# Kernel optimization log

Measured on AMD Instinct MI355X. Metric: run time of the kernel, lower is better.

Reference implementation:

```python
import jax, jax.numpy as jnp
import numpy as np

D_MODEL = 768
D_HEAD = 64
BATCH = 2
SEQ = 4096


def setup_inputs() -> dict:
    key = jax.random.key(0)
    k1, k2, k3, k4, k5 = jax.random.split(key, 5)
    x = jax.random.normal(k1, (BATCH, SEQ, D_MODEL), dtype=jnp.float32)
    # causal mask as the module expects: (seq_len, seq_len) float, 1 where attend allowed
    mask = jnp.tril(jnp.ones((SEQ, SEQ), dtype=jnp.float32))
    # weights initialized like the module: randn / sqrt(d_model)
    scale = 1.0 / np.sqrt(D_MODEL)
    Wq = jax.random.normal(k2, (D_HEAD, D_MODEL), dtype=jnp.float32) * scale
    Wk = jax.random.normal(k3, (D_HEAD, D_MODEL), dtype=jnp.float32) * scale
    Wv = jax.random.normal(k4, (D_HEAD, D_MODEL), dtype=jnp.float32) * scale
    Wo = jax.random.normal(k5, (D_MODEL, D_HEAD), dtype=jnp.float32) * scale
    return {"x": x, "mask": mask, "Wq": Wq, "Wk": Wk, "Wv": Wv, "Wo": Wo}


def reference(x, mask, Wq, Wk, Wv, Wo):
    # q,k,v: (B, S, d_head); Linear with weight (out,in) => x @ W.T
    q = jnp.einsum('bsm,hm->bsh', x, Wq)
    k = jnp.einsum('bsm,hm->bsh', x, Wk)
    v = jnp.einsum('bsm,hm->bsh', x, Wv)
    scores = jnp.einsum('bqd,bkd->bqk', q, k) / np.sqrt(D_HEAD)  # (B,S,S)
    seq_len = x.shape[1]
    m = mask[:seq_len, :seq_len]
    # faithful to the torch code: tril(scores) - 1e10 * (1 - mask)
    scores = jnp.tril(scores) - 1e10 * (1.0 - m)
    attn = jax.nn.softmax(scores, axis=-1)
    z = jnp.einsum('bqk,bkd->bqd', attn, v)  # (B,S,d_head)
    out = jnp.einsum('bsh,mh->bsm', z, Wo)   # (B,S,d_model)
    return out
```

## Files before the change

### kernel.cpp

```cpp
#include <hip/hip_runtime.h>
#include <stdint.h>

#define SEQ 4096
#define DM 768
#define DH 64

typedef __attribute__((ext_vector_type(8))) short short8;
typedef __attribute__((ext_vector_type(4))) short short4v;
typedef __attribute__((ext_vector_type(4))) float f32x4;
typedef __attribute__((ext_vector_type(2))) uint32_t uint2v;

#define LOG2E 1.4426950408889634f

static __device__ __forceinline__ short bf16r(float f) {
  union { float f; uint32_t u; } v; v.f = f;
  uint32_t u = v.u;
  return (short)((u + 0x7FFFu + ((u >> 16) & 1u)) >> 16);
}

static __device__ __forceinline__ float bf16f(uint16_t u) {
  union { uint32_t u; float f; } v; v.u = ((uint32_t)u) << 16;
  return v.f;
}

static __device__ __forceinline__ uint32_t cvtpk(float a, float b) {
  uint32_t r;
  asm("v_cvt_pk_bf16_f32 %0, %1, %2" : "=v"(r) : "v"(a), "v"(b));
  return r;
}

static __device__ __forceinline__ int swz(int row, int b) {
  return row * 128 + (b ^ ((row & 7) << 4));
}

__global__ __launch_bounds__(256) void qkv_proj(
    const float* __restrict__ x, const float* __restrict__ Wq,
    const float* __restrict__ Wk, const float* __restrict__ Wv,
    uint16_t* __restrict__ qg, uint16_t* __restrict__ kg, uint16_t* __restrict__ vg) {
  __shared__ char smem[49152] __attribute__((aligned(16)));
  const int tid = threadIdx.x;
  const int lane = tid & 63, wv = tid >> 6;
  const int l15 = lane & 15, l4 = lane >> 4;
  const int row0 = blockIdx.x * 32;
  const int nh = blockIdx.y;

  const int xr = tid >> 4, xc4 = tid & 15;
  const int mh = wv & 1, ng = wv >> 1;
  const int wr0 = tid >> 3, wb16 = tid & 7;

  const float* xp0 = x + (size_t)(row0 + xr) * DM + xc4 * 4;
  const float* xp1 = x + (size_t)(row0 + 16 + xr) * DM + xc4 * 4;

  const float* wp[3];
  int wlds[3];
  #pragma unroll
  for (int i = 0; i < 3; ++i) {
    int grow = nh * 96 + wr0 + i * 32;
    wp[i] = (grow < 64) ? (Wq + (size_t)grow * DM)
          : (grow < 128) ? (Wk + (size_t)(grow - 64) * DM)
                         : (Wv + (size_t)(grow - 128) * DM);
    wlds[i] = 4096 + swz(wr0 + i * 32, wb16 * 16);
  }
  const int xlds0 = swz(xr, xc4 * 8), xlds1 = swz(xr + 16, xc4 * 8);

  f32x4 acc[3];
  #pragma unroll
  for (int j = 0; j < 3; ++j) acc[j] = (f32x4){0.f, 0.f, 0.f, 0.f};

  float4 xA0, xA1, xB0, xB1;
  float4 wA[3][2], wB[3][2];

#define ISSUE_A(K0)                                                              \
  { xA0 = *(const float4*)(xp0 + (K0)); xA1 = *(const float4*)(xp1 + (K0));      \
    _Pragma("unroll")                                                            \
    for (int i = 0; i < 3; ++i) {                                                \
      wA[i][0] = *(const float4*)(wp[i] + (K0) + wb16 * 8);                      \
      wA[i][1] = *(const float4*)(wp[i] + (K0) + wb16 * 8 + 4);                  \
    }                                                                            \
    __builtin_amdgcn_sched_barrier(0); }
#define ISSUE_B(K0)                                                              \
  { xB0 = *(const float4*)(xp0 + (K0)); xB1 = *(const float4*)(xp1 + (K0));      \
    _Pragma("unroll")                                                            \
    for (int i = 0; i < 3; ++i) {                                                \
      wB[i][0] = *(const float4*)(wp[i] + (K0) + wb16 * 8);                      \
      wB[i][1] = *(const float4*)(wp[i] + (K0) + wb16 * 8 + 4);                  \
    }                                                                            \
    __builtin_amdgcn_sched_barrier(0); }
#define WRITE_SET(X0, X1, WS, BUF)                                               \
  { char* base_ = smem + (BUF) * 16384;                                          \
    uint2v p0 = { cvtpk(X0.x, X0.y), cvtpk(X0.z, X0.w) };                        \
    *(uint2v*)(base_ + xlds0) = p0;                                              \
    uint2v p1 = { cvtpk(X1.x, X1.y), cvtpk(X1.z, X1.w) };                        \
    *(uint2v*)(base_ + xlds1) = p1;                                              \
    _Pragma("unroll")                                                            \
    for (int i = 0; i < 3; ++i) {                                                \
      union { uint32_t u[4]; short8 s; } pk;                                     \
      pk.u[0] = cvtpk(WS[i][0].x, WS[i][0].y);                                   \
      pk.u[1] = cvtpk(WS[i][0].z, WS[i][0].w);                                   \
      pk.u[2] = cvtpk(WS[i][1].x, WS[i][1].y);                                   \
      pk.u[3] = cvtpk(WS[i][1].z, WS[i][1].w);                                   \
      *(short8*)(base_ + wlds[i]) = pk.s;                                        \
    } }
#define COMPUTE(BUF)                                                             \
  { char* base_ = smem + (BUF) * 16384;                                          \
    _Pragma("unroll")                                                            \
    for (int kc = 0; kc < 2; ++kc) {                                             \
      short8 af = *(const short8*)(base_ + swz(mh * 16 + l15, kc * 64 + l4 * 16)); \
      _Pragma("unroll")                                                          \
      for (int j = 0; j < 3; ++j) {                                              \
        int tl = ng * 3 + j;                                                     \
        short8 bfv = *(const short8*)(base_ + 4096 +                             \
                                      swz(tl * 16 + l15, kc * 64 + l4 * 16));    \
        acc[j] = __builtin_amdgcn_mfma_f32_16x16x32_bf16(af, bfv, acc[j], 0, 0, 0); \
      }                                                                          \
    } }
#define QSTEP(T, IS, X0, X1, WS, BUFW)                                           \
  { asm volatile("s_waitcnt lgkmcnt(0)" ::: "memory");                           \
    __builtin_amdgcn_s_barrier();                                                \
    if ((T) < 10) { IS(((T) + 2) * 64); }                                        \
    COMPUTE((T) % 3);                                                            \
    if ((T) < 11) { WRITE_SET(X0, X1, WS, (BUFW)); } }

  ISSUE_A(0);
  ISSUE_B(64);
  WRITE_SET(xA0, xA1, wA, 0);

  QSTEP(0,  ISSUE_A, xB0, xB1, wB, 1);
  QSTEP(1,  ISSUE_B, xA0, xA1, wA, 2);
  QSTEP(2,  ISSUE_A, xB0, xB1, wB, 0);
  QSTEP(3,  ISSUE_B, xA0, xA1, wA, 1);
  QSTEP(4,  ISSUE_A, xB0, xB1, wB, 2);
  QSTEP(5,  ISSUE_B, xA0, xA1, wA, 0);
  QSTEP(6,  ISSUE_A, xB0, xB1, wB, 1);
  QSTEP(7,  ISSUE_B, xA0, xA1, wA, 2);
  QSTEP(8,  ISSUE_A, xB0, xB1, wB, 0);
  QSTEP(9,  ISSUE_B, xA0, xA1, wA, 1);
  QSTEP(10, ISSUE_A, xB0, xB1, wB, 2);
  QSTEP(11, ISSUE_B, xA0, xA1, wA, 0);
#undef ISSUE_A
#undef ISSUE_B
#undef WRITE_SET
#undef COMPUTE
#undef QSTEP

  #pragma unroll
  for (int j = 0; j < 3; ++j) {
    int NT = nh * 6 + ng * 3 + j;
    uint16_t* dst = (NT < 4) ? qg : (NT < 8) ? kg : vg;
    const float sc = (NT < 4) ? (0.125f * LOG2E) : 1.0f;
    int cb = (NT & 3) * 16 + l15;
    #pragma unroll
    for (int r = 0; r < 4; ++r) {
      int row = row0 + mh * 16 + l4 * 4 + r;
      dst[(size_t)row * DH + cb] = (uint16_t)bf16r(acc[j][r] * sc);
    }
  }
}

__global__ __launch_bounds__(256) void attn_split(
    const uint16_t* __restrict__ qg, const uint16_t* __restrict__ kg,
    const uint16_t* __restrict__ vg, uint16_t* __restrict__ zg,
    uint16_t* __restrict__ Opart, float* __restrict__ Ml, int CHUNK, int MAXCH) {
  __shared__ char smem[32768] __attribute__((aligned(16)));

  const int tid = threadIdx.x;
  const int lane = tid & 63, wv = tid >> 6;
  const int l15 = lane & 15, l4 = lane >> 4;
  const int qt = blockIdx.x, ch = blockIdx.y, b = blockIdx.z;
  const int q0 = qt << 6;
  const int kv_lim = q0 + 64;
  const int kv_begin = ch * CHUNK;
  if (kv_begin >= kv_lim) return;
  const int kv_end = min(kv_begin + CHUNK, kv_lim);
  const int ntiles = (kv_end - kv_begin) >> 6;

  const uint16_t* qb = qg + (size_t)b * SEQ * DH;
  const uint16_t* kb = kg + (size_t)b * SEQ * DH;
  const uint16_t* vb = vg + (size_t)b * SEQ * DH;

  const int qrow = q0 + wv * 16 + l15;
  short8 qf0 = *(const short8*)(qb + (size_t)qrow * DH + l4 * 8);
  short8 qf1 = *(const short8*)(qb + (size_t)qrow * DH + 32 + l4 * 8);

  int koffA[4], koffB[4], voffA[4], voffB[4];
  #pragma unroll
  for (int n = 0; n < 4; ++n) {
    koffA[n] = swz(n * 16 + l15, l4 * 16);
    koffB[n] = swz(n * 16 + l15, 64 + l4 * 16);
    int dr = n * 16 + l15;
    voffA[n] = 8192 + dr * 128 + ((l4 * 16) ^ ((dr & 7) << 4));
    voffB[n] = 8192 + dr * 128 + ((64 + l4 * 16) ^ ((dr & 7) << 4));
  }

  const int ku = tid - 128;
  const int kvgV = tid >> 4, dqV = tid & 15;
  short8 sreg[4];
  short4v vr8[8];
  int soff[4], vwoff[4];
  if (tid >= 128) {
    #pragma unroll
    for (int i = 0; i < 4; ++i) {
      int c = ku + (i << 7);
      soff[i] = swz(c >> 3, (c & 7) * 16);
    }
  } else {
    #pragma unroll
    for (int c = 0; c < 4; ++c)
      vwoff[c] = 8192 + swz(dqV * 4 + c, kvgV * 16);
  }

#define LOAD_REGS(KV0)                                                               \
  if (tid >= 128) {                                                                  \
    _Pragma("unroll")                                                                \
    for (int i = 0; i < 4; ++i) {                                                    \
      int c = ku + (i << 7);                                                         \
      sreg[i] = *(const short8*)(kb + (size_t)((KV0) + (c >> 3)) * DH + (c & 7) * 8);  \
    }                                                                                \
  } else {                                                                           \
    _Pragma("unroll")                                                                \
    for (int i = 0; i < 8; ++i)                                                      \
      vr8[i] = *(const short4v*)(vb + (size_t)((KV0) + kvgV * 8 + i) * DH + dqV * 4);  \
  }

#define STAGE_WRITE(BUF)                                                             \
  {                                                                                  \
    char* base_ = smem + ((BUF) << 14);                                              \
    if (tid >= 128) {                                                                \
      _Pragma("unroll")                                                              \
      for (int i = 0; i < 4; ++i) *(short8*)(base_ + soff[i]) = sreg[i];             \
    } else {                                                                         \
      _Pragma("unroll")                                                              \
      for (int c = 0; c < 4; ++c) {                                                  \
        short8 w;                                                                    \
        _Pragma("unroll")                                                            \
        for (int i = 0; i < 8; ++i) w[i] = vr8[i][c];                                \
        *(short8*)(base_ + vwoff[c]) = w;                                            \
      }                                                                              \
    }                                                                                \
  }

  LOAD_REGS(kv_begin);
  STAGE_WRITE(0);

  f32x4 oaccT[4];
  #pragma unroll
  for (int n = 0; n < 4; ++n) oaccT[n] = (f32x4){0.f, 0.f, 0.f, 0.f};
  float lrun = 0.f;

  const int bp0 = (((l4 & 1) << 5) + l15) << 2;
  const int bp1 = bp0 + 64;
  const bool hi2 = (l4 >> 1) != 0;

  for (int T = 0; T < ntiles; ++T) {
    const int kv0 = kv_begin + (T << 6);
    const bool more = (T + 1 < ntiles);
    if (more) { LOAD_REGS(kv0 + 64); }
    __syncthreads();
    char* cb_ = smem + ((T & 1) << 14);

    f32x4 sacc[4];
    #pragma unroll
    for (int n = 0; n < 4; ++n) sacc[n] = (f32x4){0.f, 0.f, 0.f, 0.f};
    __builtin_amdgcn_s_setprio(1);
    #pragma unroll
    for (int n = 0; n < 4; ++n) {
      short8 kf0 = *(const short8*)(cb_ + koffA[n]);
      sacc[n] = __builtin_amdgcn_mfma_f32_16x16x32_bf16(kf0, qf0, sacc[n], 0, 0, 0);
      short8 kf1 = *(const short8*)(cb_ + koffB[n]);
      sacc[n] = __builtin_amdgcn_mfma_f32_16x16x32_bf16(kf1, qf1, sacc[n], 0, 0, 0);
    }
    __builtin_amdgcn_s_setprio(0);

    if (more) { STAGE_WRITE((T + 1) & 1); }

    if (kv0 + 63 > q0) {
      #pragma unroll
      for (int n = 0; n < 4; ++n) {
        #pragma unroll
        for (int r = 0; r < 4; ++r) {
          int kvg_ = kv0 + n * 16 + l4 * 4 + r;
          if (kvg_ > qrow) sacc[n][r] = -1e30f;
        }
      }
    }

    float ls = 0.f;
    #pragma unroll
    for (int n = 0; n < 4; ++n) {
      #pragma unroll
      for (int r = 0; r < 4; ++r) {
        float p = __builtin_amdgcn_exp2f(sacc[n][r]);
        sacc[n][r] = p;
        ls += p;
      }
    }
    ls += __shfl_xor(ls, 16);
    ls += __shfl_xor(ls, 32);
    lrun += ls;

    uint32_t pk[8];
    #pragma unroll
    for (int n = 0; n < 4; ++n) {
      pk[n * 2]     = cvtpk(sacc[n][0], sacc[n][1]);
      pk[n * 2 + 1] = cvtpk(sacc[n][2], sacc[n][3]);
    }
    union { uint32_t d[4]; short8 s; } pa0u, pa1u;
    {
      uint32_t x0 = __builtin_amdgcn_ds_bpermute(bp0, (int)pk[0]);
      uint32_t x2 = __builtin_amdgcn_ds_bpermute(bp0, (int)pk[2]);
      pa0u.d[0] = hi2 ? x2 : x0;
      uint32_t y1 = __builtin_amdgcn_ds_bpermute(bp0, (int)pk[1]);
      uint32_t y3 = __builtin_amdgcn_ds_bpermute(bp0, (int)pk[3]);
      pa0u.d[1] = hi2 ? y3 : y1;
      uint32_t z0 = __builtin_amdgcn_ds_bpermute(bp1, (int)pk[0]);
      uint32_t z2 = __builtin_amdgcn_ds_bpermute(bp1, (int)pk[2]);
      pa0u.d[2] = hi2 ? z2 : z0;
      uint32_t w1 = __builtin_amdgcn_ds_bpermute(bp1, (int)pk[1]);
      uint32_t w3 = __builtin_amdgcn_ds_bpermute(bp1, (int)pk[3]);
      pa0u.d[3] = hi2 ? w3 : w1;
      uint32_t x4 = __builtin_amdgcn_ds_bpermute(bp0, (int)pk[4]);
      uint32_t x6 = __builtin_amdgcn_ds_bpermute(bp0, (int)pk[6]);
      pa1u.d[0] = hi2 ? x6 : x4;
      uint32_t y5 = __builtin_amdgcn_ds_bpermute(bp0, (int)pk[5]);
      uint32_t y7 = __builtin_amdgcn_ds_bpermute(bp0, (int)pk[7]);
      pa1u.d[1] = hi2 ? y7 : y5;
      uint32_t z4 = __builtin_amdgcn_ds_bpermute(bp1, (int)pk[4]);
      uint32_t z6 = __builtin_amdgcn_ds_bpermute(bp1, (int)pk[6]);
      pa1u.d[2] = hi2 ? z6 : z4;
      uint32_t w5 = __builtin_amdgcn_ds_bpermute(bp1, (int)pk[5]);
      uint32_t w7 = __builtin_amdgcn_ds_bpermute(bp1, (int)pk[7]);
      pa1u.d[3] = hi2 ? w7 : w5;
    }
    __builtin_amdgcn_s_setprio(1);
    #pragma unroll
    for (int n = 0; n < 4; ++n) {
      short8 vf0 = *(const short8*)(cb_ + voffA[n]);
      oaccT[n] = __builtin_amdgcn_mfma_f32_16x16x32_bf16(vf0, pa0u.s, oaccT[n], 0, 0, 0);
      short8 vf1 = *(const short8*)(cb_ + voffB[n]);
      oaccT[n] = __builtin_amdgcn_mfma_f32_16x16x32_bf16(vf1, pa1u.s, oaccT[n], 0, 0, 0);
    }
    __builtin_amdgcn_s_setprio(0);
  }
#undef LOAD_REGS
#undef STAGE_WRITE

  const int rl = wv * 16 + l15;
  if (MAXCH == 1) {
    float invl = 1.0f / lrun;
    uint16_t* zb = zg + (size_t)b * SEQ * DH;
    #pragma unroll
    for (int n = 0; n < 4; ++n) {
      short4v pkv = { bf16r(oaccT[n][0] * invl), bf16r(oaccT[n][1] * invl),
                      bf16r(oaccT[n][2] * invl), bf16r(oaccT[n][3] * invl) };
      *(short4v*)(zb + (size_t)(q0 + rl) * DH + n * 16 + l4 * 4) = pkv;
    }
  } else {
    const size_t slot = ((size_t)(b << 6) + qt) * MAXCH + ch;
    uint16_t* op = Opart + slot * 4096;
    #pragma unroll
    for (int n = 0; n < 4; ++n) {
      short4v pkv = { bf16r(oaccT[n][0]), bf16r(oaccT[n][1]),
                      bf16r(oaccT[n][2]), bf16r(oaccT[n][3]) };
      *(short4v*)(op + (size_t)rl * 64 + n * 16 + l4 * 4) = pkv;
    }
    if (l4 == 0) Ml[slot * 64 + rl] = lrun;
  }
}

__global__ __launch_bounds__(256) void out_proj(
    const uint16_t* __restrict__ Opart, const float* __restrict__ Ml,
    const uint16_t* __restrict__ zg, const float* __restrict__ Wo,
    float* __restrict__ out, int CHUNK, int MAXCH) {
  __shared__ char smem[4096 + 32768] __attribute__((aligned(16)));
  char* Zl = smem;
  char* Wl = smem + 4096;
  const int tid = threadIdx.x;
  const int lane = tid & 63, wv = tid >> 6;
  const int l15 = lane & 15, l4 = lane >> 4;
  const int row0 = blockIdx.x * 32;
  const int col0 = blockIdx.y * 256;

  {
    const int r = tid >> 3, c0 = (tid & 7) << 3;
    if (MAXCH == 1) {
      short8 v = *(const short8*)(zg + (size_t)(row0 + r) * DH + c0);
      *(short8*)(Zl + swz(r, c0 * 2)) = v;
    } else {
      const int b = row0 >> 12;
      const int rlb = row0 & 4095;
      const int qt = rlb >> 6, q0 = qt << 6;
      const int row_local = (rlb & 63) + r;
      const int nch = (q0 + 64 + CHUNK - 1) / CHUNK;
      const size_t sbase = ((size_t)(b << 6) + qt) * MAXCH;
      float a[8] = {0.f, 0.f, 0.f, 0.f, 0.f, 0.f, 0.f, 0.f};
      float wsum = 0.f;
      for (int ch = 0; ch < nch; ++ch) {
        const size_t s = sbase + ch;
        wsum += Ml[s * 64 + row_local];
        short8 v = *(const short8*)(Opart + s * 4096 + (size_t)row_local * 64 + c0);
        #pragma unroll
        for (int j = 0; j < 8; ++j) a[j] += bf16f((uint16_t)v[j]);
      }
      float inv = 1.0f / wsum;
      short8 pk;
      #pragma unroll
      for (int j = 0; j < 8; ++j) pk[j] = bf16r(a[j] * inv);
      *(short8*)(Zl + swz(r, c0 * 2)) = pk;
    }
  }
  #pragma unroll
  for (int i = 0; i < 16; ++i) {
    int id = tid + (i << 8);
    int m = id >> 4, c4 = id & 15;
    float4 vw = *(const float4*)(Wo + (size_t)(col0 + m) * DH + c4 * 4);
    uint2v pk = { cvtpk(vw.x, vw.y), cvtpk(vw.z, vw.w) };
    *(uint2v*)(Wl + swz(m, c4 * 8)) = pk;
  }
  __syncthreads();

  const int mh = wv & 1, ng = wv >> 1;
  short8 af0 = *(const short8*)(Zl + swz(mh * 16 + l15, l4 * 16));
  short8 af1 = *(const short8*)(Zl + swz(mh * 16 + l15, 64 + l4 * 16));
  f32x4 acc[8];
  #pragma unroll
  for (int j = 0; j < 8; ++j) acc[j] = (f32x4){0.f, 0.f, 0.f, 0.f};
  #pragma unroll
  for (int j = 0; j < 8; ++j) {
    int nt = ng * 8 + j;
    short8 b0 = *(const short8*)(Wl + swz(nt * 16 + l15, l4 * 16));
    acc[j] = __builtin_amdgcn_mfma_f32_16x16x32_bf16(af0, b0, acc[j], 0, 0, 0);
    short8 b1 = *(const short8*)(Wl + swz(nt * 16 + l15, 64 + l4 * 16));
    acc[j] = __builtin_amdgcn_mfma_f32_16x16x32_bf16(af1, b1, acc[j], 0, 0, 0);
  }
  #pragma unroll
  for (int j = 0; j < 8; ++j) {
    int nt = ng * 8 + j;
    #pragma unroll
    for (int r = 0; r < 4; ++r) {
      int row = row0 + mh * 16 + l4 * 4 + r;
      int col = col0 + nt * 16 + l15;
      out[(size_t)row * DM + col] = acc[j][r];
    }
  }
}

extern "C" void kernel_launch(void* const* d_in, const int* in_sizes, int n_in,
                              void* d_out, int out_size, void* d_ws, size_t ws_size,
                              hipStream_t stream) {
  const float* x  = (const float*)d_in[0];
  const float* Wq = (const float*)d_in[2];
  const float* Wk = (const float*)d_in[3];
  const float* Wv = (const float*)d_in[4];
  const float* Wo = (const float*)d_in[5];
  float* out = (float*)d_out;

  const size_t N = (size_t)2 * SEQ * DH;
  uint16_t* qg = (uint16_t*)d_ws;
  uint16_t* kg = qg + N;
  uint16_t* vg = kg + N;
  uint16_t* zg = vg + N;
  uint16_t* Opart = zg + N;

  int maxch = 16;
  while (maxch > 1) {
    size_t slots = (size_t)2 * 64 * maxch;
    size_t need = 4 * N * 2 + slots * (4096 * 2 + 64 * 4);
    if (need <= ws_size) break;
    maxch >>= 1;
  }
  const int CHUNK = SEQ / maxch;
  float* Ml = (float*)(Opart + (size_t)2 * 64 * maxch * 4096);

  qkv_proj<<<dim3(256, 2), 256, 0, stream>>>(x, Wq, Wk, Wv, qg, kg, vg);
  attn_split<<<dim3(64, maxch, 2), 256, 0, stream>>>(qg, kg, vg, zg, Opart, Ml,
                                                     CHUNK, maxch);
  out_proj<<<dim3(256, 3), 256, 0, stream>>>(Opart, Ml, zg, Wo, out, CHUNK, maxch);
}
```

Before: 46.99 us.

## Process two 64-row query tiles per attention block to share K/V tiles

```diff
diff --git a/kernel.cpp b/kernel.cpp
--- a/kernel.cpp
+++ b/kernel.cpp
@@ -31,6 +31,37 @@
 
 static __device__ __forceinline__ int swz(int row, int b) {
   return row * 128 + (b ^ ((row & 7) << 4));
+}
+
+static __device__ __forceinline__ void redist(const uint32_t* pk, int bp0, int bp1,
+                                              bool hi2, short8& pa0s, short8& pa1s) {
+  union { uint32_t d[4]; short8 s; } pa0u, pa1u;
+  uint32_t x0 = __builtin_amdgcn_ds_bpermute(bp0, (int)pk[0]);
+  uint32_t x2 = __builtin_amdgcn_ds_bpermute(bp0, (int)pk[2]);
+  pa0u.d[0] = hi2 ? x2 : x0;
+  uint32_t y1 = __builtin_amdgcn_ds_bpermute(bp0, (int)pk[1]);
+  uint32_t y3 = __builtin_amdgcn_ds_bpermute(bp0, (int)pk[3]);
+  pa0u.d[1] = hi2 ? y3 : y1;
+  uint32_t z0 = __builtin_amdgcn_ds_bpermute(bp1, (int)pk[0]);
+  uint32_t z2 = __builtin_amdgcn_ds_bpermute(bp1, (int)pk[2]);
+  pa0u.d[2] = hi2 ? z2 : z0;
+  uint32_t w1 = __builtin_amdgcn_ds_bpermute(bp1, (int)pk[1]);
+  uint32_t w3 = __builtin_amdgcn_ds_bpermute(bp1, (int)pk[3]);
+  pa0u.d[3] = hi2 ? w3 : w1;
+  uint32_t x4 = __builtin_amdgcn_ds_bpermute(bp0, (int)pk[4]);
+  uint32_t x6 = __builtin_amdgcn_ds_bpermute(bp0, (int)pk[6]);
+  pa1u.d[0] = hi2 ? x6 : x4;
+  uint32_t y5 = __builtin_amdgcn_ds_bpermute(bp0, (int)pk[5]);
+  uint32_t y7 = __builtin_amdgcn_ds_bpermute(bp0, (int)pk[7]);
+  pa1u.d[1] = hi2 ? y7 : y5;
+  uint32_t z4 = __builtin_amdgcn_ds_bpermute(bp1, (int)pk[4]);
+  uint32_t z6 = __builtin_amdgcn_ds_bpermute(bp1, (int)pk[6]);
+  pa1u.d[2] = hi2 ? z6 : z4;
+  uint32_t w5 = __builtin_amdgcn_ds_bpermute(bp1, (int)pk[5]);
+  uint32_t w7 = __builtin_amdgcn_ds_bpermute(bp1, (int)pk[7]);
+  pa1u.d[3] = hi2 ? w7 : w5;
+  pa0s = pa0u.s;
+  pa1s = pa1u.s;
 }
 
 __global__ __launch_bounds__(256) void qkv_proj(
@@ -167,8 +198,8 @@
   const int lane = tid & 63, wv = tid >> 6;
   const int l15 = lane & 15, l4 = lane >> 4;
   const int qt = blockIdx.x, ch = blockIdx.y, b = blockIdx.z;
-  const int q0 = qt << 6;
-  const int kv_lim = q0 + 64;
+  const int q0 = qt << 7;
+  const int kv_lim = q0 + 128;
   const int kv_begin = ch * CHUNK;
   if (kv_begin >= kv_lim) return;
   const int kv_end = min(kv_begin + CHUNK, kv_lim);
@@ -178,9 +209,12 @@
   const uint16_t* kb = kg + (size_t)b * SEQ * DH;
   const uint16_t* vb = vg + (size_t)b * SEQ * DH;
 
-  const int qrow = q0 + wv * 16 + l15;
-  short8 qf0 = *(const short8*)(qb + (size_t)qrow * DH + l4 * 8);
-  short8 qf1 = *(const short8*)(qb + (size_t)qrow * DH + 32 + l4 * 8);
+  const int qrowA = q0 + wv * 16 + l15;
+  const int qrowB = qrowA + 64;
+  short8 qfA0 = *(const short8*)(qb + (size_t)qrowA * DH + l4 * 8);
+  short8 qfA1 = *(const short8*)(qb + (size_t)qrowA * DH + 32 + l4 * 8);
+  short8 qfB0 = *(const short8*)(qb + (size_t)qrowB * DH + l4 * 8);
+  short8 qfB1 = *(const short8*)(qb + (size_t)qrowB * DH + 32 + l4 * 8);
 
   int koffA[4], koffB[4], voffA[4], voffB[4];
   #pragma unroll
@@ -242,10 +276,13 @@
   LOAD_REGS(kv_begin);
   STAGE_WRITE(0);
 
-  f32x4 oaccT[4];
-  #pragma unroll
-  for (int n = 0; n < 4; ++n) oaccT[n] = (f32x4){0.f, 0.f, 0.f, 0.f};
-  float lrun = 0.f;
+  f32x4 oaccA[4], oaccB[4];
+  #pragma unroll
+  for (int n = 0; n < 4; ++n) {
+    oaccA[n] = (f32x4){0.f, 0.f, 0.f, 0.f};
+    oaccB[n] = (f32x4){0.f, 0.f, 0.f, 0.f};
+  }
+  float lrunA = 0.f, lrunB = 0.f;
 
   const int bp0 = (((l4 & 1) << 5) + l15) << 2;
   const int bp1 = bp0 + 64;
@@ -258,16 +295,21 @@
     __syncthreads();
     char* cb_ = smem + ((T & 1) << 14);
 
-    f32x4 sacc[4];
-    #pragma unroll
-    for (int n = 0; n < 4; ++n) sacc[n] = (f32x4){0.f, 0.f, 0.f, 0.f};
+    f32x4 saccA[4], saccB[4];
+    #pragma unroll
+    for (int n = 0; n < 4; ++n) {
+      saccA[n] = (f32x4){0.f, 0.f, 0.f, 0.f};
+      saccB[n] = (f32x4){0.f, 0.f, 0.f, 0.f};
+    }
     __builtin_amdgcn_s_setprio(1);
     #pragma unroll
     for (int n = 0; n < 4; ++n) {
       short8 kf0 = *(const short8*)(cb_ + koffA[n]);
-      sacc[n] = __builtin_amdgcn_mfma_f32_16x16x32_bf16(kf0, qf0, sacc[n], 0, 0, 0);
       short8 kf1 = *(const short8*)(cb_ + koffB[n]);
-      sacc[n] = __builtin_amdgcn_mfma_f32_16x16x32_bf16(kf1, qf1, sacc[n], 0, 0, 0);
+      saccA[n] = __builtin_amdgcn_mfma_f32_16x16x32_bf16(kf0, qfA0, saccA[n], 0, 0, 0);
+      saccA[n] = __builtin_amdgcn_mfma_f32_16x16x32_bf16(kf1, qfA1, saccA[n], 0, 0, 0);
+      saccB[n] = __builtin_amdgcn_mfma_f32_16x16x32_bf16(kf0, qfB0, saccB[n], 0, 0, 0);
+      saccB[n] = __builtin_amdgcn_mfma_f32_16x16x32_bf16(kf1, qfB1, saccB[n], 0, 0, 0);
     }
     __builtin_amdgcn_s_setprio(0);
 
@@ -279,65 +321,53 @@
         #pragma unroll
         for (int r = 0; r < 4; ++r) {
           int kvg_ = kv0 + n * 16 + l4 * 4 + r;
-          if (kvg_ > qrow) sacc[n][r] = -1e30f;
+          if (kvg_ > qrowA) saccA[n][r] = -1e30f;
+          if (kvg_ > qrowB) saccB[n][r] = -1e30f;
         }
       }
     }
 
-    float ls = 0.f;
+    float lsA = 0.f, lsB = 0.f;
     #pragma unroll
     for (int n = 0; n < 4; ++n) {
       #pragma unroll
       for (int r = 0; r < 4; ++r) {
-        float p = __builtin_amdgcn_exp2f(sacc[n][r]);
-        sacc[n][r] = p;
-        ls += p;
+        float pA = __builtin_amdgcn_exp2f(saccA[n][r]);
+        float pB = __builtin_amdgcn_exp2f(saccB[n][r]);
+        saccA[n][r] = pA;
+        saccB[n][r] = pB;
+        lsA += pA;
+        lsB += pB;
       }
     }
-    ls += __shfl_xor(ls, 16);
-    ls += __shfl_xor(ls, 32);
-    lrun += ls;
-
-    uint32_t pk[8];
-    #pragma unroll
-    for (int n = 0; n < 4; ++n) {
-      pk[n * 2]     = cvtpk(sacc[n][0], sacc[n][1]);
-      pk[n * 2 + 1] = cvtpk(sacc[n][2], sacc[n][3]);
-    }
-    union { uint32_t d[4]; short8 s; } pa0u, pa1u;
-    {
-      uint32_t x0 = __builtin_amdgcn_ds_bpermute(bp0, (int)pk[0]);
-      uint32_t x2 = __builtin_amdgcn_ds_bpermute(bp0, (int)pk[2]);
-      pa0u.d[0] = hi2 ? x2 : x0;
-      uint32_t y1 = __builtin_amdgcn_ds_bpermute(bp0, (int)pk[1]);
-      uint32_t y3 = __builtin_amdgcn_ds_bpermute(bp0, (int)pk[3]);
-      pa0u.d[1] = hi2 ? y3 : y1;
-      uint32_t z0 = __builtin_amdgcn_ds_bpermute(bp1, (int)pk[0]);
-      uint32_t z2 = __builtin_amdgcn_ds_bpermute(bp1, (int)pk[2]);
-      pa0u.d[2] = hi2 ? z2 : z0;
-      uint32_t w1 = __builtin_amdgcn_ds_bpermute(bp1, (int)pk[1]);
-      uint32_t w3 = __builtin_amdgcn_ds_bpermute(bp1, (int)pk[3]);
-      pa0u.d[3] = hi2 ? w3 : w1;
-      uint32_t x4 = __builtin_amdgcn_ds_bpermute(bp0, (int)pk[4]);
-      uint32_t x6 = __builtin_amdgcn_ds_bpermute(bp0, (int)pk[6]);
-      pa1u.d[0] = hi2 ? x6 : x4;
-      uint32_t y5 = __builtin_amdgcn_ds_bpermute(bp0, (int)pk[5]);
-      uint32_t y7 = __builtin_amdgcn_ds_bpermute(bp0, (int)pk[7]);
-      pa1u.d[1] = hi2 ? y7 : y5;
-      uint32_t z4 = __builtin_amdgcn_ds_bpermute(bp1, (int)pk[4]);
-      uint32_t z6 = __builtin_amdgcn_ds_bpermute(bp1, (int)pk[6]);
-      pa1u.d[2] = hi2 ? z6 : z4;
-      uint32_t w5 = __builtin_amdgcn_ds_bpermute(bp1, (int)pk[5]);
-      uint32_t w7 = __builtin_amdgcn_ds_bpermute(bp1, (int)pk[7]);
-      pa1u.d[3] = hi2 ? w7 : w5;
-    }
+    lsA += __shfl_xor(lsA, 16);
+    lsA += __shfl_xor(lsA, 32);
+    lsB += __shfl_xor(lsB, 16);
+    lsB += __shfl_xor(lsB, 32);
+    lrunA += lsA;
+    lrunB += lsB;
+
+    uint32_t pkA[8], pkB[8];
+    #pragma unroll
+    for (int n = 0; n < 4; ++n) {
+      pkA[n * 2]     = cvtpk(saccA[n][0], saccA[n][1]);
+      pkA[n * 2 + 1] = cvtpk(saccA[n][2], saccA[n][3]);
+      pkB[n * 2]     = cvtpk(saccB[n][0], saccB[n][1]);
+      pkB[n * 2 + 1] = cvtpk(saccB[n][2], saccB[n][3]);
+    }
+    short8 paA0, paA1, paB0, paB1;
+    redist(pkA, bp0, bp1, hi2, paA0, paA1);
+    redist(pkB, bp0, bp1, hi2, paB0, paB1);
+
     __builtin_amdgcn_s_setprio(1);
     #pragma unroll
     for (int n = 0; n < 4; ++n) {
       short8 vf0 = *(const short8*)(cb_ + voffA[n]);
-      oaccT[n] = __builtin_amdgcn_mfma_f32_16x16x32_bf16(vf0, pa0u.s, oaccT[n], 0, 0, 0);
       short8 vf1 = *(const short8*)(cb_ + voffB[n]);
-      oaccT[n] = __builtin_amdgcn_mfma_f32_16x16x32_bf16(vf1, pa1u.s, oaccT[n], 0, 0, 0);
+      oaccA[n] = __builtin_amdgcn_mfma_f32_16x16x32_bf16(vf0, paA0, oaccA[n], 0, 0, 0);
+      oaccA[n] = __builtin_amdgcn_mfma_f32_16x16x32_bf16(vf1, paA1, oaccA[n], 0, 0, 0);
+      oaccB[n] = __builtin_amdgcn_mfma_f32_16x16x32_bf16(vf0, paB0, oaccB[n], 0, 0, 0);
+      oaccB[n] = __builtin_amdgcn_mfma_f32_16x16x32_bf16(vf1, paB1, oaccB[n], 0, 0, 0);
     }
     __builtin_amdgcn_s_setprio(0);
   }
@@ -346,24 +376,35 @@
 
   const int rl = wv * 16 + l15;
   if (MAXCH == 1) {
-    float invl = 1.0f / lrun;
+    float invA = 1.0f / lrunA, invB = 1.0f / lrunB;
     uint16_t* zb = zg + (size_t)b * SEQ * DH;
     #pragma unroll
     for (int n = 0; n < 4; ++n) {
-      short4v pkv = { bf16r(oaccT[n][0] * invl), bf16r(oaccT[n][1] * invl),
-                      bf16r(oaccT[n][2] * invl), bf16r(oaccT[n][3] * invl) };
-      *(short4v*)(zb + (size_t)(q0 + rl) * DH + n * 16 + l4 * 4) = pkv;
+      short4v pA = { bf16r(oaccA[n][0] * invA), bf16r(oaccA[n][1] * invA),
+                     bf16r(oaccA[n][2] * invA), bf16r(oaccA[n][3] * invA) };
+      *(short4v*)(zb + (size_t)(q0 + rl) * DH + n * 16 + l4 * 4) = pA;
+      short4v pB = { bf16r(oaccB[n][0] * invB), bf16r(oaccB[n][1] * invB),
+                     bf16r(oaccB[n][2] * invB), bf16r(oaccB[n][3] * invB) };
+      *(short4v*)(zb + (size_t)(q0 + 64 + rl) * DH + n * 16 + l4 * 4) = pB;
     }
   } else {
-    const size_t slot = ((size_t)(b << 6) + qt) * MAXCH + ch;
-    uint16_t* op = Opart + slot * 4096;
-    #pragma unroll
-    for (int n = 0; n < 4; ++n) {
-      short4v pkv = { bf16r(oaccT[n][0]), bf16r(oaccT[n][1]),
-                      bf16r(oaccT[n][2]), bf16r(oaccT[n][3]) };
-      *(short4v*)(op + (size_t)rl * 64 + n * 16 + l4 * 4) = pkv;
-    }
-    if (l4 == 0) Ml[slot * 64 + rl] = lrun;
+    const size_t slotA = ((size_t)(b << 6) + (qt << 1)) * MAXCH + ch;
+    const size_t slotB = slotA + MAXCH;
+    uint16_t* opA = Opart + slotA * 4096;
+    uint16_t* opB = Opart + slotB * 4096;
+    #pragma unroll
+    for (int n = 0; n < 4; ++n) {
+      short4v pA = { bf16r(oaccA[n][0]), bf16r(oaccA[n][1]),
+                     bf16r(oaccA[n][2]), bf16r(oaccA[n][3]) };
+      *(short4v*)(opA + (size_t)rl * 64 + n * 16 + l4 * 4) = pA;
+      short4v pB = { bf16r(oaccB[n][0]), bf16r(oaccB[n][1]),
+                     bf16r(oaccB[n][2]), bf16r(oaccB[n][3]) };
+      *(short4v*)(opB + (size_t)rl * 64 + n * 16 + l4 * 4) = pB;
+    }
+    if (l4 == 0) {
+      Ml[slotA * 64 + rl] = lrunA;
+      Ml[slotB * 64 + rl] = lrunB;
+    }
   }
 }
 
@@ -472,7 +513,7 @@
   float* Ml = (float*)(Opart + (size_t)2 * 64 * maxch * 4096);
 
   qkv_proj<<<dim3(256, 2), 256, 0, stream>>>(x, Wq, Wk, Wv, qg, kg, vg);
-  attn_split<<<dim3(64, maxch, 2), 256, 0, stream>>>(qg, kg, vg, zg, Opart, Ml,
+  attn_split<<<dim3(32, maxch, 2), 256, 0, stream>>>(qg, kg, vg, zg, Opart, Ml,
                                                      CHUNK, maxch);
   out_proj<<<dim3(256, 3), 256, 0, stream>>>(Opart, Ml, zg, Wo, out, CHUNK, maxch);
 }
```

Measured after the change: 50.64 us. 1.08x slower.
